# Kernel optimization log

Hardware: AMD Instinct MI355X
Metric: run time of the kernel (lower is better)

## Reference

```python
import jax, jax.numpy as jnp
import numpy as np

N_EMBD = 1024
N_HEAD = 16
N_CTX = 2048
HEAD_DIM = N_EMBD // N_HEAD


def setup_inputs() -> dict:
    key = jax.random.key(0)
    k1, k2, k3 = jax.random.split(key, 3)
    B, S = 4, 2048
    inputs = jax.random.normal(k1, (B, S, N_EMBD), dtype=jnp.float32)
    # Conv1D weights: stored as (d_in, d_out), init std=0.02, zero bias
    w_attn = jax.random.normal(k2, (N_EMBD, 3 * N_EMBD), dtype=jnp.float32) * 0.02
    b_attn = jnp.zeros((3 * N_EMBD,), dtype=jnp.float32)
    w_proj = jax.random.normal(k3, (N_EMBD, N_EMBD), dtype=jnp.float32) * 0.02
    b_proj = jnp.zeros((N_EMBD,), dtype=jnp.float32)
    return {"inputs": inputs, "w_attn": w_attn, "b_attn": b_attn,
            "w_proj": w_proj, "b_proj": b_proj}


def reference(inputs, w_attn, b_attn, w_proj, b_proj):
    B, S, E = inputs.shape
    H, D = N_HEAD, HEAD_DIM
    # qkv projection (Conv1D == Linear with transposed weight)
    qkv = inputs @ w_attn + b_attn                      # [B,S,3E]
    q, k, v = jnp.split(qkv, 3, axis=-1)
    q = q.reshape(B, S, H, D).transpose(0, 2, 1, 3)     # [B,H,S,D]
    k = k.reshape(B, S, H, D).transpose(0, 2, 1, 3)
    v = v.reshape(B, S, H, D).transpose(0, 2, 1, 3)
    # scores = Q K^T / sqrt(D) (scale=True)
    scores = jnp.einsum('bhqd,bhkd->bhqk', q, k) / jnp.float32(D) ** 0.5
    # GPT-2 style causal bias: scores*bias - 10000*(1-bias)
    bias = jnp.tril(jnp.ones((S, S), dtype=scores.dtype))[None, None]
    scores = scores * bias - 10000.0 * (1.0 - bias)
    attn = jax.nn.softmax(scores, axis=-1)
    out = jnp.einsum('bhqk,bhkd->bhqd', attn, v)        # [B,H,S,D]
    out = out.transpose(0, 2, 1, 3).reshape(B, S, E)    # merge heads
    return out @ w_proj + b_proj
```

## Files before the change

kernel.cpp:

```cpp
#include <hip/hip_runtime.h>
#include <hip/hip_bf16.h>
#include <stdint.h>

typedef __bf16 bf16x8 __attribute__((ext_vector_type(8)));
typedef float f32x4 __attribute__((ext_vector_type(4)));
typedef float f32x16 __attribute__((ext_vector_type(16)));
typedef uint32_t u32x4 __attribute__((ext_vector_type(4)));

#define B_SZ 4
#define S_CTX 2048
#define EMB 1024
#define NH 16
#define HD 64
#define BH_TOT (B_SZ * NH)
#define QSCALE 0.18033688f

__device__ __forceinline__ uint16_t f2bf(float f) {
    uint32_t u = __builtin_bit_cast(uint32_t, f);
    u += 0x7FFF + ((u >> 16) & 1);
    return (uint16_t)(u >> 16);
}

__device__ __forceinline__ uint32_t pk2bf(float lo, float hi) {
    uint32_t a = __builtin_bit_cast(uint32_t, lo);
    uint32_t b = __builtin_bit_cast(uint32_t, hi);
    a += 0x7FFF + ((a >> 16) & 1);
    b += 0x7FFF + ((b >> 16) & 1);
    return __builtin_amdgcn_perm(b, a, 0x07060302);
}

__device__ __forceinline__ void async16(const uint16_t* g, uint16_t* l) {
    __builtin_amdgcn_global_load_lds(
        (const __attribute__((address_space(1))) uint32_t*)g,
        (__attribute__((address_space(3))) uint32_t*)l, 16, 0, 0);
}

__global__ __launch_bounds__(256) void cvt_kernel(const float* __restrict__ in,
                                                  uint16_t* __restrict__ out, int n) {
    int i = (blockIdx.x * 256 + threadIdx.x) * 4;
    int stride = gridDim.x * 256 * 4;
    for (; i < n; i += stride) {
        float4 v = *(const float4*)(in + i);
        ushort4 o;
        o.x = f2bf(v.x); o.y = f2bf(v.y); o.z = f2bf(v.z); o.w = f2bf(v.w);
        *(ushort4*)(out + i) = o;
    }
}

__global__ __launch_bounds__(1024) void transpose_kernel(const float* __restrict__ in,
                                                         uint16_t* __restrict__ out,
                                                         int R, int C) {
    __shared__ float tile[32][33];
    int tx = threadIdx.x, ty = threadIdx.y;
    int c0 = blockIdx.x * 32, r0 = blockIdx.y * 32;
    tile[ty][tx] = in[(size_t)(r0 + ty) * C + c0 + tx];
    __syncthreads();
    out[(size_t)(c0 + ty) * R + r0 + tx] = f2bf(tile[tx][ty]);
}

template <int MODE>
__global__ __launch_bounds__(256) void gemm_bt(
    const uint16_t* __restrict__ A, const uint16_t* __restrict__ Bt,
    const float* __restrict__ bias,
    uint16_t* __restrict__ oQ, uint16_t* __restrict__ oK, uint16_t* __restrict__ oV,
    float* __restrict__ oF, int M, int N, int K) {
    __shared__ uint16_t As[128 * 32];
    __shared__ uint16_t Bs[128 * 32];
    int t = threadIdx.x;
    int m0 = blockIdx.y * 128, n0 = blockIdx.x * 128;
    int l = t & 63, w = t >> 6;
    int wr = w >> 1, wc = w & 1;
    int lr = l & 15, lk = l >> 4;

    int srow = l >> 2;
    int scol = (l & 3) * 8;
    const uint16_t* gA0 = A + (size_t)(m0 + w * 16 + srow) * K + scol;
    const uint16_t* gA1 = A + (size_t)(m0 + (w + 4) * 16 + srow) * K + scol;
    const uint16_t* gB0 = Bt + (size_t)(n0 + w * 16 + srow) * K + scol;
    const uint16_t* gB1 = Bt + (size_t)(n0 + (w + 4) * 16 + srow) * K + scol;
    uint16_t* lA0 = As + w * 512;
    uint16_t* lA1 = As + (w + 4) * 512;
    uint16_t* lB0 = Bs + w * 512;
    uint16_t* lB1 = Bs + (w + 4) * 512;

    f32x4 acc[4][4];
#pragma unroll
    for (int i = 0; i < 4; ++i)
#pragma unroll
        for (int j = 0; j < 4; ++j) acc[i][j] = (f32x4){0.f, 0.f, 0.f, 0.f};

    for (int k0 = 0; k0 < K; k0 += 32) {
        async16(gA0 + k0, lA0);
        async16(gA1 + k0, lA1);
        async16(gB0 + k0, lB0);
        async16(gB1 + k0, lB1);
        __syncthreads();
        bf16x8 af[4], bf[4];
#pragma unroll
        for (int i = 0; i < 4; ++i)
            af[i] = *(const bf16x8*)(As + (wr * 64 + i * 16 + lr) * 32 + lk * 8);
#pragma unroll
        for (int j = 0; j < 4; ++j)
            bf[j] = *(const bf16x8*)(Bs + (wc * 64 + j * 16 + lr) * 32 + lk * 8);
#pragma unroll
        for (int i = 0; i < 4; ++i)
#pragma unroll
            for (int j = 0; j < 4; ++j)
                acc[i][j] = __builtin_amdgcn_mfma_f32_16x16x32_bf16(af[i], bf[j], acc[i][j], 0, 0, 0);
        __syncthreads();
    }

#pragma unroll
    for (int i = 0; i < 4; ++i) {
        int rowb = m0 + wr * 64 + i * 16 + lk * 4;
#pragma unroll
        for (int j = 0; j < 4; ++j) {
            int col = n0 + wc * 64 + j * 16 + lr;
            float bv = bias[col];
            if (MODE == 0) {
                int sect = col >> 10;
                int hd = col & 1023;
                int h = hd >> 6, d = hd & 63;
                int b = rowb >> 11, s = rowb & 2047;
                int bh = b * NH + h;
                if (sect == 0) {
#pragma unroll
                    for (int r = 0; r < 4; ++r)
                        oQ[((size_t)bh * S_CTX + s + r) * HD + d] =
                            f2bf((acc[i][j][r] + bv) * QSCALE);
                } else if (sect == 1) {
#pragma unroll
                    for (int r = 0; r < 4; ++r)
                        oK[((size_t)bh * S_CTX + s + r) * HD + d] = f2bf(acc[i][j][r] + bv);
                } else {
                    ushort4 v4;
                    v4.x = f2bf(acc[i][j][0] + bv);
                    v4.y = f2bf(acc[i][j][1] + bv);
                    v4.z = f2bf(acc[i][j][2] + bv);
                    v4.w = f2bf(acc[i][j][3] + bv);
                    *(ushort4*)(oV + ((size_t)bh * HD + d) * S_CTX + s) = v4;
                }
            } else {
#pragma unroll
                for (int r = 0; r < 4; ++r) {
                    int row = rowb + r;
                    oF[(size_t)row * N + col] = acc[i][j][r] + bv;
                }
            }
        }
    }
}

template <bool MASKED>
__device__ __forceinline__ void attn_compute(
    int lq, const bf16x8 (&qf)[4], const bf16x8 (&kf)[4], const bf16x8 (&vf)[4],
    int hi, f32x16& accO0, f32x16& accO1, float& lsum) {
    f32x16 s = {};
#pragma unroll
    for (int t = 0; t < 4; ++t)
        s = __builtin_amdgcn_mfma_f32_32x32x16_bf16(kf[t], qf[t], s, 0, 0, 0);
    float p[16];
    float ps = 0.f;
#pragma unroll
    for (int r = 0; r < 16; ++r) {
        float e = exp2f(s[r]);
        if (MASKED) {
            int kvr = (r & 3) + 8 * (r >> 2) + 4 * hi;
            e = (kvr > lq) ? 0.f : e;
        }
        p[r] = e;
        ps += e;
    }
    lsum += ps;
    uint32_t pw[8];
#pragma unroll
    for (int g = 0; g < 2; ++g) {
        uint32_t x0 = pk2bf(p[8 * g + 0], p[8 * g + 1]);
        uint32_t y0 = pk2bf(p[8 * g + 4], p[8 * g + 5]);
        asm("v_permlane32_swap_b32 %0, %1" : "+v"(x0), "+v"(y0));
        uint32_t x1 = pk2bf(p[8 * g + 2], p[8 * g + 3]);
        uint32_t y1 = pk2bf(p[8 * g + 6], p[8 * g + 7]);
        asm("v_permlane32_swap_b32 %0, %1" : "+v"(x1), "+v"(y1));
        pw[4 * g + 0] = x0; pw[4 * g + 1] = x1; pw[4 * g + 2] = y0; pw[4 * g + 3] = y1;
    }
    bf16x8 pa0 = __builtin_bit_cast(bf16x8, (u32x4){pw[0], pw[1], pw[2], pw[3]});
    bf16x8 pa1 = __builtin_bit_cast(bf16x8, (u32x4){pw[4], pw[5], pw[6], pw[7]});
    accO0 = __builtin_amdgcn_mfma_f32_32x32x16_bf16(pa0, vf[0], accO0, 0, 0, 0);
    accO0 = __builtin_amdgcn_mfma_f32_32x32x16_bf16(pa1, vf[1], accO0, 0, 0, 0);
    accO1 = __builtin_amdgcn_mfma_f32_32x32x16_bf16(pa0, vf[2], accO1, 0, 0, 0);
    accO1 = __builtin_amdgcn_mfma_f32_32x32x16_bf16(pa1, vf[3], accO1, 0, 0, 0);
}

__global__ __launch_bounds__(256) void attn32_kernel(
    const uint16_t* __restrict__ Q, const uint16_t* __restrict__ Kc,
    const uint16_t* __restrict__ Vt, uint16_t* __restrict__ AO) {
    __shared__ float lbuf[4][32];
    int blk = blockIdx.x;
    int v = (blk & 7) * 128 + (blk >> 3);
    int bh = v >> 4, ii = v & 15;
    int w = threadIdx.x >> 6, l = threadIdx.x & 63;
    int tile = (w == 0) ? ii : (w == 1) ? 31 - ii : (w == 2) ? 32 + ii : 63 - ii;
    int lq = l & 31, hi = l >> 5;
    const uint16_t* Qh = Q + (size_t)bh * S_CTX * HD;
    const uint16_t* Kh = Kc + (size_t)bh * S_CTX * HD;
    const uint16_t* Vh = Vt + (size_t)bh * HD * S_CTX;
    int q0 = tile * 32;

    bf16x8 qf[4];
#pragma unroll
    for (int t = 0; t < 4; ++t)
        qf[t] = *(const bf16x8*)(Qh + (q0 + lq) * HD + t * 16 + hi * 8);

    f32x16 accO0 = {}, accO1 = {};
    float lsum = 0.f;

    bf16x8 kf[4], vf[4], kn[4], vn[4];
#pragma unroll
    for (int t = 0; t < 4; ++t)
        kf[t] = *(const bf16x8*)(Kh + (size_t)lq * HD + t * 16 + hi * 8);
    vf[0] = *(const bf16x8*)(Vh + (size_t)lq * S_CTX + hi * 8);
    vf[1] = *(const bf16x8*)(Vh + (size_t)lq * S_CTX + 16 + hi * 8);
    vf[2] = *(const bf16x8*)(Vh + (size_t)(32 + lq) * S_CTX + hi * 8);
    vf[3] = *(const bf16x8*)(Vh + (size_t)(32 + lq) * S_CTX + 16 + hi * 8);

    for (int kvt = 0; kvt < tile; ++kvt) {
        int kv1 = (kvt + 1) * 32;
#pragma unroll
        for (int t = 0; t < 4; ++t)
            kn[t] = *(const bf16x8*)(Kh + (size_t)(kv1 + lq) * HD + t * 16 + hi * 8);
        vn[0] = *(const bf16x8*)(Vh + (size_t)lq * S_CTX + kv1 + hi * 8);
        vn[1] = *(const bf16x8*)(Vh + (size_t)lq * S_CTX + kv1 + 16 + hi * 8);
        vn[2] = *(const bf16x8*)(Vh + (size_t)(32 + lq) * S_CTX + kv1 + hi * 8);
        vn[3] = *(const bf16x8*)(Vh + (size_t)(32 + lq) * S_CTX + kv1 + 16 + hi * 8);
        attn_compute<false>(lq, qf, kf, vf, hi, accO0, accO1, lsum);
#pragma unroll
        for (int t = 0; t < 4; ++t) { kf[t] = kn[t]; vf[t] = vn[t]; }
    }
    attn_compute<true>(lq, qf, kf, vf, hi, accO0, accO1, lsum);

    float lt = lsum + __shfl_xor(lsum, 32);
    lbuf[w][lq] = lt;
    asm volatile("s_waitcnt lgkmcnt(0)" ::: "memory");
    int b = bh >> 4, h = bh & 15;
#pragma unroll
    for (int r = 0; r < 16; ++r) {
        int qr = q0 + (r & 3) + 8 * (r >> 2) + 4 * hi;
        float inv = 1.f / lbuf[w][(r & 3) + 8 * (r >> 2) + 4 * hi];
        AO[((size_t)(b * S_CTX + qr)) * EMB + h * HD + lq] = f2bf(accO0[r] * inv);
        AO[((size_t)(b * S_CTX + qr)) * EMB + h * HD + 32 + lq] = f2bf(accO1[r] * inv);
    }
}

extern "C" void kernel_launch(void* const* d_in, const int* in_sizes, int n_in,
                              void* d_out, int out_size, void* d_ws, size_t ws_size,
                              hipStream_t stream) {
    const float* x = (const float*)d_in[0];
    const float* w_attn = (const float*)d_in[1];
    const float* b_attn = (const float*)d_in[2];
    const float* w_proj = (const float*)d_in[3];
    const float* b_proj = (const float*)d_in[4];
    float* out = (float*)d_out;
    char* ws = (char*)d_ws;

    uint16_t* Xb  = (uint16_t*)(ws);
    uint16_t* WaT = (uint16_t*)(ws + (16ull << 20));
    uint16_t* WpT = (uint16_t*)(ws + (22ull << 20));
    uint16_t* Qb  = (uint16_t*)(ws + (24ull << 20));
    uint16_t* Kb  = (uint16_t*)(ws + (40ull << 20));
    uint16_t* Vt  = (uint16_t*)(ws + (56ull << 20));
    uint16_t* AO  = (uint16_t*)(ws + (72ull << 20));

    cvt_kernel<<<2048, 256, 0, stream>>>(x, Xb, B_SZ * S_CTX * EMB);
    transpose_kernel<<<dim3(3 * EMB / 32, EMB / 32), dim3(32, 32), 0, stream>>>(w_attn, WaT, EMB, 3 * EMB);
    transpose_kernel<<<dim3(EMB / 32, EMB / 32), dim3(32, 32), 0, stream>>>(w_proj, WpT, EMB, EMB);
    gemm_bt<0><<<dim3(3 * EMB / 128, (B_SZ * S_CTX) / 128), 256, 0, stream>>>(
        Xb, WaT, b_attn, Qb, Kb, Vt, nullptr, B_SZ * S_CTX, 3 * EMB, EMB);
    attn32_kernel<<<BH_TOT * 16, 256, 0, stream>>>(Qb, Kb, Vt, AO);
    gemm_bt<1><<<dim3(EMB / 128, (B_SZ * S_CTX) / 128), 256, 0, stream>>>(
        AO, WpT, b_proj, nullptr, nullptr, nullptr, out, B_SZ * S_CTX, EMB, EMB);
}
```

Baseline: 333.4 us.

## Share K/V tiles across waves via double-buffered swizzled LDS with contiguous query tiles

Each block now handles four consecutive 32-row query tiles of one head, so its four waves can share K/V tiles. K and V are staged cooperatively into double-buffered, XOR-swizzled LDS instead of each wave loading its own K/V from global memory. This cuts redundant global/L2 traffic by up to 4x. In exchange it adds two barriers per KV step, waves whose diagonal comes earlier sit idle until the last wave finishes, and the old per-block causal load balancing across tiles ii/31-ii/32+ii/63-ii is dropped.

```diff
diff --git a/kernel.cpp b/kernel.cpp
--- a/kernel.cpp
+++ b/kernel.cpp
@@ -194,49 +194,81 @@
 __global__ __launch_bounds__(256) void attn32_kernel(
     const uint16_t* __restrict__ Q, const uint16_t* __restrict__ Kc,
     const uint16_t* __restrict__ Vt, uint16_t* __restrict__ AO) {
+    __shared__ uint16_t Klds[2][32 * 64];
+    __shared__ uint16_t Vlds[2][64 * 32];
     __shared__ float lbuf[4][32];
     int blk = blockIdx.x;
-    int v = (blk & 7) * 128 + (blk >> 3);
-    int bh = v >> 4, ii = v & 15;
-    int w = threadIdx.x >> 6, l = threadIdx.x & 63;
-    int tile = (w == 0) ? ii : (w == 1) ? 31 - ii : (w == 2) ? 32 + ii : 63 - ii;
+    int xcd = blk & 7, j = blk >> 3;
+    int bh = xcd * 8 + (j >> 4);
+    int gi = 15 - (j & 15);
+    int tid = threadIdx.x;
+    int w = tid >> 6, l = tid & 63;
+    int mytile = gi * 4 + w;
+    int last = gi * 4 + 3;
     int lq = l & 31, hi = l >> 5;
     const uint16_t* Qh = Q + (size_t)bh * S_CTX * HD;
     const uint16_t* Kh = Kc + (size_t)bh * S_CTX * HD;
     const uint16_t* Vh = Vt + (size_t)bh * HD * S_CTX;
-    int q0 = tile * 32;
+    int q0 = mytile * 32;
 
     bf16x8 qf[4];
 #pragma unroll
     for (int t = 0; t < 4; ++t)
         qf[t] = *(const bf16x8*)(Qh + (q0 + lq) * HD + t * 16 + hi * 8);
 
+    int ksr = tid >> 3, ksc = tid & 7;
+    int ksw = ksr * 128 + ((ksc ^ (ksr & 7)) << 4);
+    const uint16_t* kg = Kh + ksr * HD + ksc * 8;
+    int vsr = tid >> 2, vsc = tid & 3;
+    int vsw = vsr * 64 + ((vsc ^ (vsr & 3)) << 4);
+    const uint16_t* vg = Vh + (size_t)vsr * S_CTX + vsc * 8;
+
+    int kro = lq * 128;
+    int vro0 = lq * 64, vro1 = (32 + lq) * 64;
+    int ksz = lq & 7, vsz = lq & 3;
+
     f32x16 accO0 = {}, accO1 = {};
     float lsum = 0.f;
 
-    bf16x8 kf[4], vf[4], kn[4], vn[4];
-#pragma unroll
-    for (int t = 0; t < 4; ++t)
-        kf[t] = *(const bf16x8*)(Kh + (size_t)lq * HD + t * 16 + hi * 8);
-    vf[0] = *(const bf16x8*)(Vh + (size_t)lq * S_CTX + hi * 8);
-    vf[1] = *(const bf16x8*)(Vh + (size_t)lq * S_CTX + 16 + hi * 8);
-    vf[2] = *(const bf16x8*)(Vh + (size_t)(32 + lq) * S_CTX + hi * 8);
-    vf[3] = *(const bf16x8*)(Vh + (size_t)(32 + lq) * S_CTX + 16 + hi * 8);
-
-    for (int kvt = 0; kvt < tile; ++kvt) {
-        int kv1 = (kvt + 1) * 32;
-#pragma unroll
-        for (int t = 0; t < 4; ++t)
-            kn[t] = *(const bf16x8*)(Kh + (size_t)(kv1 + lq) * HD + t * 16 + hi * 8);
-        vn[0] = *(const bf16x8*)(Vh + (size_t)lq * S_CTX + kv1 + hi * 8);
-        vn[1] = *(const bf16x8*)(Vh + (size_t)lq * S_CTX + kv1 + 16 + hi * 8);
-        vn[2] = *(const bf16x8*)(Vh + (size_t)(32 + lq) * S_CTX + kv1 + hi * 8);
-        vn[3] = *(const bf16x8*)(Vh + (size_t)(32 + lq) * S_CTX + kv1 + 16 + hi * 8);
-        attn_compute<false>(lq, qf, kf, vf, hi, accO0, accO1, lsum);
-#pragma unroll
-        for (int t = 0; t < 4; ++t) { kf[t] = kn[t]; vf[t] = vn[t]; }
-    }
-    attn_compute<true>(lq, qf, kf, vf, hi, accO0, accO1, lsum);
+    {
+        uint4 kr = *(const uint4*)kg;
+        uint4 vr = *(const uint4*)vg;
+        *(uint4*)((char*)Klds[0] + ksw) = kr;
+        *(uint4*)((char*)Vlds[0] + vsw) = vr;
+    }
+    __syncthreads();
+
+    for (int kvt = 0; kvt <= last; ++kvt) {
+        uint4 kr, vr;
+        bool stage = (kvt < last);
+        if (stage) {
+            kr = *(const uint4*)(kg + (size_t)(kvt + 1) * 32 * HD);
+            vr = *(const uint4*)(vg + (kvt + 1) * 32);
+        }
+        if (kvt <= mytile) {
+            const char* kb = (const char*)Klds[kvt & 1];
+            const char* vb = (const char*)Vlds[kvt & 1];
+            bf16x8 kf[4], vf[4];
+#pragma unroll
+            for (int t = 0; t < 4; ++t)
+                kf[t] = *(const bf16x8*)(kb + kro + (((2 * t + hi) ^ ksz) << 4));
+            vf[0] = *(const bf16x8*)(vb + vro0 + ((hi ^ vsz) << 4));
+            vf[1] = *(const bf16x8*)(vb + vro0 + (((2 + hi) ^ vsz) << 4));
+            vf[2] = *(const bf16x8*)(vb + vro1 + ((hi ^ vsz) << 4));
+            vf[3] = *(const bf16x8*)(vb + vro1 + (((2 + hi) ^ vsz) << 4));
+            if (kvt == mytile)
+                attn_compute<true>(lq, qf, kf, vf, hi, accO0, accO1, lsum);
+            else
+                attn_compute<false>(lq, qf, kf, vf, hi, accO0, accO1, lsum);
+        }
+        __syncthreads();
+        if (stage) {
+            int p = (kvt + 1) & 1;
+            *(uint4*)((char*)Klds[p] + ksw) = kr;
+            *(uint4*)((char*)Vlds[p] + vsw) = vr;
+        }
+        __syncthreads();
+    }
 
     float lt = lsum + __shfl_xor(lsum, 32);
     lbuf[w][lq] = lt;
```

Measured after the change: 326.8 us. 2.0% less time.

## Write K and V in MFMA-fragment-tiled layout for coalesced attention loads

Applied to the files above, without the earlier changes.

The QKV projection epilogue now stores K and V in a per-32-key tiled layout that matches the MFMA operand fragments, so each lane of the attention kernel reads contiguous 16-byte chunks at lane*8 offsets. Before, these loads were strided rows of K and transposed V. This is meant to coalesce the global loads in the attention inner loop and simplify address arithmetic. Separately, the bf16 packing for P drops round-to-nearest-even and uses plain round-half-up, which saves a few ALU ops at a small cost in rounding accuracy. The epilogue stores in the GEMM become more scattered, which may cost some time there.

```diff
diff --git a/kernel.cpp b/kernel.cpp
--- a/kernel.cpp
+++ b/kernel.cpp
@@ -22,10 +22,8 @@
 }
 
 __device__ __forceinline__ uint32_t pk2bf(float lo, float hi) {
-    uint32_t a = __builtin_bit_cast(uint32_t, lo);
-    uint32_t b = __builtin_bit_cast(uint32_t, hi);
-    a += 0x7FFF + ((a >> 16) & 1);
-    b += 0x7FFF + ((b >> 16) & 1);
+    uint32_t a = __builtin_bit_cast(uint32_t, lo) + 0x8000;
+    uint32_t b = __builtin_bit_cast(uint32_t, hi) + 0x8000;
     return __builtin_amdgcn_perm(b, a, 0x07060302);
 }
 
@@ -129,16 +127,21 @@
                         oQ[((size_t)bh * S_CTX + s + r) * HD + d] =
                             f2bf((acc[i][j][r] + bv) * QSCALE);
                 } else if (sect == 1) {
+                    size_t kbase = (size_t)bh * (S_CTX * HD) + (size_t)(s >> 5) * 2048 +
+                                   (d >> 4) * 512 + ((d >> 3) & 1) * 256 + (s & 31) * 8 + (d & 7);
 #pragma unroll
                     for (int r = 0; r < 4; ++r)
-                        oK[((size_t)bh * S_CTX + s + r) * HD + d] = f2bf(acc[i][j][r] + bv);
+                        oK[kbase + r * 8] = f2bf(acc[i][j][r] + bv);
                 } else {
+                    size_t vbase = (size_t)bh * (S_CTX * HD) + (size_t)(s >> 5) * 2048 +
+                                   ((d >> 5) * 2 + ((s >> 4) & 1)) * 512 +
+                                   (((s >> 3) & 1) * 32 + (d & 31)) * 8 + (s & 7);
                     ushort4 v4;
                     v4.x = f2bf(acc[i][j][0] + bv);
                     v4.y = f2bf(acc[i][j][1] + bv);
                     v4.z = f2bf(acc[i][j][2] + bv);
                     v4.w = f2bf(acc[i][j][3] + bv);
-                    *(ushort4*)(oV + ((size_t)bh * HD + d) * S_CTX + s) = v4;
+                    *(ushort4*)(oV + vbase) = v4;
                 }
             } else {
 #pragma unroll
@@ -192,8 +195,8 @@
 }
 
 __global__ __launch_bounds__(256) void attn32_kernel(
-    const uint16_t* __restrict__ Q, const uint16_t* __restrict__ Kc,
-    const uint16_t* __restrict__ Vt, uint16_t* __restrict__ AO) {
+    const uint16_t* __restrict__ Q, const uint16_t* __restrict__ Kf,
+    const uint16_t* __restrict__ Vf, uint16_t* __restrict__ AO) {
     __shared__ float lbuf[4][32];
     int blk = blockIdx.x;
     int v = (blk & 7) * 128 + (blk >> 3);
@@ -202,8 +205,8 @@
     int tile = (w == 0) ? ii : (w == 1) ? 31 - ii : (w == 2) ? 32 + ii : 63 - ii;
     int lq = l & 31, hi = l >> 5;
     const uint16_t* Qh = Q + (size_t)bh * S_CTX * HD;
-    const uint16_t* Kh = Kc + (size_t)bh * S_CTX * HD;
-    const uint16_t* Vh = Vt + (size_t)bh * HD * S_CTX;
+    const uint16_t* kb = Kf + (size_t)bh * (S_CTX * HD) + l * 8;
+    const uint16_t* vb = Vf + (size_t)bh * (S_CTX * HD) + l * 8;
     int q0 = tile * 32;
 
     bf16x8 qf[4];
@@ -216,22 +219,16 @@
 
     bf16x8 kf[4], vf[4], kn[4], vn[4];
 #pragma unroll
-    for (int t = 0; t < 4; ++t)
-        kf[t] = *(const bf16x8*)(Kh + (size_t)lq * HD + t * 16 + hi * 8);
-    vf[0] = *(const bf16x8*)(Vh + (size_t)lq * S_CTX + hi * 8);
-    vf[1] = *(const bf16x8*)(Vh + (size_t)lq * S_CTX + 16 + hi * 8);
-    vf[2] = *(const bf16x8*)(Vh + (size_t)(32 + lq) * S_CTX + hi * 8);
-    vf[3] = *(const bf16x8*)(Vh + (size_t)(32 + lq) * S_CTX + 16 + hi * 8);
+    for (int t = 0; t < 4; ++t) kf[t] = *(const bf16x8*)(kb + t * 512);
+#pragma unroll
+    for (int t = 0; t < 4; ++t) vf[t] = *(const bf16x8*)(vb + t * 512);
 
     for (int kvt = 0; kvt < tile; ++kvt) {
-        int kv1 = (kvt + 1) * 32;
-#pragma unroll
-        for (int t = 0; t < 4; ++t)
-            kn[t] = *(const bf16x8*)(Kh + (size_t)(kv1 + lq) * HD + t * 16 + hi * 8);
-        vn[0] = *(const bf16x8*)(Vh + (size_t)lq * S_CTX + kv1 + hi * 8);
-        vn[1] = *(const bf16x8*)(Vh + (size_t)lq * S_CTX + kv1 + 16 + hi * 8);
-        vn[2] = *(const bf16x8*)(Vh + (size_t)(32 + lq) * S_CTX + kv1 + hi * 8);
-        vn[3] = *(const bf16x8*)(Vh + (size_t)(32 + lq) * S_CTX + kv1 + 16 + hi * 8);
+        size_t nb = (size_t)(kvt + 1) * 2048;
+#pragma unroll
+        for (int t = 0; t < 4; ++t) kn[t] = *(const bf16x8*)(kb + nb + t * 512);
+#pragma unroll
+        for (int t = 0; t < 4; ++t) vn[t] = *(const bf16x8*)(vb + nb + t * 512);
         attn_compute<false>(lq, qf, kf, vf, hi, accO0, accO1, lsum);
 #pragma unroll
         for (int t = 0; t < 4; ++t) { kf[t] = kn[t]; vf[t] = vn[t]; }
```

Measured after the change: 287.4 us. -13.8%, faster.
